# Performance work log

Hardware: AMD Instinct MI355X
Metric: run time of the kernel (lower is better)

Reference implementation:

```python
import jax, jax.numpy as jnp
import numpy as np

N = 200000      # number of nodes / samples
D = 256         # embedding_dim
K = 20          # n_clusters


def setup_inputs() -> dict:
    key = jax.random.key(0)
    k1, k2 = jax.random.split(key)
    embeddings = jax.random.normal(k1, (N, D), dtype=jnp.float32)
    # indicator P has orthonormal-ish columns in the original (top-k eigenvectors
    # of ZZ^T); random values are fine for a correctness baseline of the math.
    indicator = jax.random.normal(k2, (N, K), dtype=jnp.float32)
    return {"embeddings": embeddings, "indicator": indicator}


def reference(embeddings, indicator):
    # Jc = tr(Z Z^T) - tr(P^T Z Z^T P)
    # tr(Z Z^T) = sum(Z * Z)
    term1 = jnp.sum(embeddings * embeddings)
    # tr(P^T Z Z^T P) = || Z^T P ||_F^2 ; Z^T P is [D, K] (tiny), avoids N x N gram.
    ztp = jnp.einsum('nd,nk->dk', embeddings, indicator)
    term2 = jnp.sum(ztp * ztp)
    return term1 - term2
```

## Files before the change

### kernel.cpp

```cpp
#include <hip/hip_runtime.h>

#define NN 200000
#define DD 256
#define KK 20

__global__ __launch_bounds__(512) void egac_main(
    const float* __restrict__ Z, const float* __restrict__ P,
    float* __restrict__ ztp_part, float* __restrict__ t1_part, int chunk) {
  const int t = threadIdx.x;
  const int c2 = t & 127;
  const int r = t >> 7;
  const int b = blockIdx.x;
  const int base = b * chunk;
  int rows = NN - base;
  if (rows > chunk) rows = chunk;

  float acc0[KK], acc1[KK];
#pragma unroll
  for (int k = 0; k < KK; ++k) { acc0[k] = 0.f; acc1[k] = 0.f; }
  float t1 = 0.f;

  const float2* Zb = (const float2*)(Z + (size_t)base * DD);

#pragma unroll 4
  for (int j = r; j < rows; j += 4) {
    float2 zv = Zb[j * (DD / 2) + c2];
    int rowu = __builtin_amdgcn_readfirstlane(base + j);
    const float4* pr = (const float4*)(P + (size_t)rowu * KK);
    float4 pa = pr[0], pb = pr[1], pc = pr[2], pd = pr[3], pe = pr[4];
    float pv[KK] = {pa.x, pa.y, pa.z, pa.w, pb.x, pb.y, pb.z, pb.w,
                    pc.x, pc.y, pc.z, pc.w, pd.x, pd.y, pd.z, pd.w,
                    pe.x, pe.y, pe.z, pe.w};
    t1 += zv.x * zv.x + zv.y * zv.y;
#pragma unroll
    for (int k = 0; k < KK; ++k) {
      acc0[k] += zv.x * pv[k];
      acc1[k] += zv.y * pv[k];
    }
  }

  __shared__ float red[KK][DD];
  __shared__ float wsum[8];
  for (int ph = 0; ph < 4; ++ph) {
    if (r == ph) {
      if (ph == 0) {
#pragma unroll
        for (int k = 0; k < KK; ++k) {
          red[k][2 * c2] = acc0[k];
          red[k][2 * c2 + 1] = acc1[k];
        }
      } else {
#pragma unroll
        for (int k = 0; k < KK; ++k) {
          red[k][2 * c2] += acc0[k];
          red[k][2 * c2 + 1] += acc1[k];
        }
      }
    }
    __syncthreads();
  }

#pragma unroll
  for (int off = 32; off > 0; off >>= 1) t1 += __shfl_xor(t1, off, 64);
  if ((t & 63) == 0) wsum[t >> 6] = t1;
  __syncthreads();

  const float* redf = &red[0][0];
#pragma unroll
  for (int i = 0; i < (KK * DD) / 512; ++i)
    ztp_part[(size_t)b * (KK * DD) + i * 512 + t] = redf[i * 512 + t];
  if (t == 0) {
    float s = 0.f;
#pragma unroll
    for (int w = 0; w < 8; ++w) s += wsum[w];
    t1_part[b] = s;
  }
}

__global__ __launch_bounds__(512) void egac_reduce(
    const float* __restrict__ ztp_part, const float* __restrict__ t1_part,
    float* __restrict__ out, int nb) {
  __shared__ float red[16][32];
  const int t = threadIdx.x;
  const int e_local = t & 31;
  const int psub = t >> 5;
  const int e = blockIdx.x * 32 + e_local;

  float s = 0.f;
#pragma unroll
  for (int j = 0; j < 16; ++j) {
    int p = psub * 16 + j;
    if (p < nb) s += ztp_part[(size_t)p * (KK * DD) + e];
  }
  red[psub][e_local] = s;
  __syncthreads();
  for (int sh = 8; sh >= 1; sh >>= 1) {
    if (psub < sh) red[psub][e_local] += red[psub + sh][e_local];
    __syncthreads();
  }
  if (t == 0) {
    float ssq = 0.f;
#pragma unroll
    for (int i = 0; i < 32; ++i) {
      float v = red[0][i];
      ssq += v * v;
    }
    atomicAdd(out, -ssq);
  }

  if (blockIdx.x == 0) {
    float v = (t < nb) ? t1_part[t] : 0.f;
#pragma unroll
    for (int off = 32; off > 0; off >>= 1) v += __shfl_xor(v, off, 64);
    __shared__ float w2[8];
    if ((t & 63) == 0) w2[t >> 6] = v;
    __syncthreads();
    if (t == 0) {
      float tt = 0.f;
#pragma unroll
      for (int w = 0; w < 8; ++w) tt += w2[w];
      atomicAdd(out, tt);
    }
  }
}

extern "C" void kernel_launch(void* const* d_in, const int* in_sizes, int n_in,
                              void* d_out, int out_size, void* d_ws,
                              size_t ws_size, hipStream_t stream) {
  const float* Z = (const float*)d_in[0];
  const float* P = (const float*)d_in[1];
  float* out = (float*)d_out;

  int nb = 256;
  size_t per_block = (size_t)KK * DD * sizeof(float) + sizeof(float);
  if (ws_size < (size_t)nb * per_block) {
    nb = (int)(ws_size / per_block);
    if (nb < 1) nb = 1;
  }
  float* ztp_part = (float*)d_ws;
  float* t1_part = (float*)d_ws + (size_t)nb * KK * DD;
  int chunk = (NN + nb - 1) / nb;

  hipMemsetAsync(d_out, 0, sizeof(float), stream);
  egac_main<<<nb, 512, 0, stream>>>(Z, P, ztp_part, t1_part, chunk);
  egac_reduce<<<160, 512, 0, stream>>>(ztp_part, t1_part, out, nb);
}
```

Before: 367.8 us.

## Software-pipeline row loads with float4 lanes and rebalance grid to more blocks

The main kernel now processes rows with 256-thread blocks where each wave handles one row using float4 loads per lane. It adds a three-stage register software pipeline that prefetches Z and P rows ahead of the FMA work, which is meant to hide global memory latency. The grid grows from 256 to 1000 blocks so more CUs are filled, and the reduce kernel gains loops to handle the larger partial count. The cost is more register pressure and a larger partial-sum buffer to reduce. The pipeline also assumes chunk divides evenly and silently clamps out-of-range rows to row 0.

After: 321.1 us. 1.15x faster.

```diff
diff --git a/kernel.cpp b/kernel.cpp
--- a/kernel.cpp
+++ b/kernel.cpp
@@ -4,56 +4,87 @@
 #define DD 256
 #define KK 20
 
-__global__ __launch_bounds__(512) void egac_main(
+
+#define STAGE_LOAD(s, zv, Q0, Q1, Q2, Q3, Q4)                              \
+  {                                                                        \
+    int j_ = base + ((s) << 2) + w;                                        \
+    if (j_ > NN - 1) j_ = 0;        \
+    zv = Zr[(size_t)j_ * (DD / 4) + lane];                                 \
+    int ru_ = __builtin_amdgcn_readfirstlane(j_);                          \
+    const float4* pp_ = (const float4*)(P + (size_t)ru_ * KK);             \
+    Q0 = pp_[0]; Q1 = pp_[1]; Q2 = pp_[2]; Q3 = pp_[3]; Q4 = pp_[4];       \
+  }
+
+#define STAGE_COMPUTE(zv, Q0, Q1, Q2, Q3, Q4)                              \
+  {                                                                        \
+    float zz_[4] = {zv.x, zv.y, zv.z, zv.w};                               \
+    float pv_[KK] = {Q0.x, Q0.y, Q0.z, Q0.w, Q1.x, Q1.y, Q1.z, Q1.w,       \
+                     Q2.x, Q2.y, Q2.z, Q2.w, Q3.x, Q3.y, Q3.z, Q3.w,       \
+                     Q4.x, Q4.y, Q4.z, Q4.w};                              \
+    t1 += zz_[0] * zz_[0] + zz_[1] * zz_[1];                               \
+    t1 += zz_[2] * zz_[2] + zz_[3] * zz_[3];                               \
+    _Pragma("unroll") for (int k_ = 0; k_ < KK; ++k_) {                    \
+      _Pragma("unroll") for (int c_ = 0; c_ < 4; ++c_)                     \
+          acc[k_][c_] += zz_[c_] * pv_[k_];                                \
+    }                                                                      \
+  }
+
+__global__ __launch_bounds__(256, 2) void egac_main(
     const float* __restrict__ Z, const float* __restrict__ P,
     float* __restrict__ ztp_part, float* __restrict__ t1_part, int chunk) {
   const int t = threadIdx.x;
-  const int c2 = t & 127;
-  const int r = t >> 7;
+  const int lane = t & 63;
+  const int w = t >> 6;
   const int b = blockIdx.x;
   const int base = b * chunk;
-  int rows = NN - base;
-  if (rows > chunk) rows = chunk;
+  const int nst = chunk >> 2;
 
-  float acc0[KK], acc1[KK];
+  float acc[KK][4];
 #pragma unroll
-  for (int k = 0; k < KK; ++k) { acc0[k] = 0.f; acc1[k] = 0.f; }
+  for (int k = 0; k < KK; ++k)
+#pragma unroll
+    for (int c = 0; c < 4; ++c) acc[k][c] = 0.f;
   float t1 = 0.f;
 
-  const float2* Zb = (const float2*)(Z + (size_t)base * DD);
+  const float4* Zr = (const float4*)Z;
 
-#pragma unroll 4
-  for (int j = r; j < rows; j += 4) {
-    float2 zv = Zb[j * (DD / 2) + c2];
-    int rowu = __builtin_amdgcn_readfirstlane(base + j);
-    const float4* pr = (const float4*)(P + (size_t)rowu * KK);
-    float4 pa = pr[0], pb = pr[1], pc = pr[2], pd = pr[3], pe = pr[4];
-    float pv[KK] = {pa.x, pa.y, pa.z, pa.w, pb.x, pb.y, pb.z, pb.w,
-                    pc.x, pc.y, pc.z, pc.w, pd.x, pd.y, pd.z, pd.w,
-                    pe.x, pe.y, pe.z, pe.w};
-    t1 += zv.x * zv.x + zv.y * zv.y;
-#pragma unroll
-    for (int k = 0; k < KK; ++k) {
-      acc0[k] += zv.x * pv[k];
-      acc1[k] += zv.y * pv[k];
-    }
+  float4 zA, A0, A1, A2, A3, A4;
+  float4 zB, B0, B1, B2, B3, B4;
+  float4 zC, C0, C1, C2, C3, C4;
+
+  STAGE_LOAD(0, zA, A0, A1, A2, A3, A4);
+  STAGE_LOAD(1, zB, B0, B1, B2, B3, B4);
+
+  int s = 0;
+  const int m_end = (nst - 2) / 3;
+  for (int m = 0; m < m_end; ++m) {
+    STAGE_LOAD(s + 2, zC, C0, C1, C2, C3, C4);
+    STAGE_COMPUTE(zA, A0, A1, A2, A3, A4);
+    STAGE_LOAD(s + 3, zA, A0, A1, A2, A3, A4);
+    STAGE_COMPUTE(zB, B0, B1, B2, B3, B4);
+    STAGE_LOAD(s + 4, zB, B0, B1, B2, B3, B4);
+    STAGE_COMPUTE(zC, C0, C1, C2, C3, C4);
+    s += 3;
   }
+  STAGE_COMPUTE(zA, A0, A1, A2, A3, A4);
+  STAGE_COMPUTE(zB, B0, B1, B2, B3, B4);
 
   __shared__ float red[KK][DD];
-  __shared__ float wsum[8];
+  __shared__ float wsum[4];
   for (int ph = 0; ph < 4; ++ph) {
-    if (r == ph) {
+    if (w == ph) {
       if (ph == 0) {
 #pragma unroll
-        for (int k = 0; k < KK; ++k) {
-          red[k][2 * c2] = acc0[k];
-          red[k][2 * c2 + 1] = acc1[k];
-        }
+        for (int k = 0; k < KK; ++k)
+          ((float4*)&red[k][0])[lane] =
+              make_float4(acc[k][0], acc[k][1], acc[k][2], acc[k][3]);
       } else {
 #pragma unroll
         for (int k = 0; k < KK; ++k) {
-          red[k][2 * c2] += acc0[k];
-          red[k][2 * c2 + 1] += acc1[k];
+          float4 r = ((float4*)&red[k][0])[lane];
+          r.x += acc[k][0]; r.y += acc[k][1];
+          r.z += acc[k][2]; r.w += acc[k][3];
+          ((float4*)&red[k][0])[lane] = r;
         }
       }
     }
@@ -62,19 +93,15 @@
 
 #pragma unroll
   for (int off = 32; off > 0; off >>= 1) t1 += __shfl_xor(t1, off, 64);
-  if ((t & 63) == 0) wsum[t >> 6] = t1;
+  if (lane == 0) wsum[w] = t1;
   __syncthreads();
 
-  const float* redf = &red[0][0];
+  float4* dst = (float4*)(ztp_part + (size_t)b * (KK * DD));
+  const float4* src = (const float4*)&red[0][0];
 #pragma unroll
-  for (int i = 0; i < (KK * DD) / 512; ++i)
-    ztp_part[(size_t)b * (KK * DD) + i * 512 + t] = redf[i * 512 + t];
-  if (t == 0) {
-    float s = 0.f;
-#pragma unroll
-    for (int w = 0; w < 8; ++w) s += wsum[w];
-    t1_part[b] = s;
-  }
+  for (int i = 0; i < (KK * DD) / (4 * 256); ++i)
+    dst[i * 256 + t] = src[i * 256 + t];
+  if (t == 0) t1_part[b] = wsum[0] + wsum[1] + wsum[2] + wsum[3];
 }
 
 __global__ __launch_bounds__(512) void egac_reduce(
@@ -82,20 +109,16 @@
     float* __restrict__ out, int nb) {
   __shared__ float red[16][32];
   const int t = threadIdx.x;
-  const int e_local = t & 31;
-  const int psub = t >> 5;
-  const int e = blockIdx.x * 32 + e_local;
+  const int el = t & 31;
+  const int ps = t >> 5;
+  const int e = blockIdx.x * 32 + el;
 
   float s = 0.f;
-#pragma unroll
-  for (int j = 0; j < 16; ++j) {
-    int p = psub * 16 + j;
-    if (p < nb) s += ztp_part[(size_t)p * (KK * DD) + e];
-  }
-  red[psub][e_local] = s;
+  for (int p = ps; p < nb; p += 16) s += ztp_part[(size_t)p * (KK * DD) + e];
+  red[ps][el] = s;
   __syncthreads();
   for (int sh = 8; sh >= 1; sh >>= 1) {
-    if (psub < sh) red[psub][e_local] += red[psub + sh][e_local];
+    if (ps < sh) red[ps][el] += red[ps + sh][el];
     __syncthreads();
   }
   if (t == 0) {
@@ -109,7 +132,8 @@
   }
 
   if (blockIdx.x == 0) {
-    float v = (t < nb) ? t1_part[t] : 0.f;
+    float v = 0.f;
+    for (int i = t; i < nb; i += 512) v += t1_part[i];
 #pragma unroll
     for (int off = 32; off > 0; off >>= 1) v += __shfl_xor(v, off, 64);
     __shared__ float w2[8];
@@ -118,7 +142,7 @@
     if (t == 0) {
       float tt = 0.f;
 #pragma unroll
-      for (int w = 0; w < 8; ++w) tt += w2[w];
+      for (int i = 0; i < 8; ++i) tt += w2[i];
       atomicAdd(out, tt);
     }
   }
@@ -131,17 +155,15 @@
   const float* P = (const float*)d_in[1];
   float* out = (float*)d_out;
 
-  int nb = 256;
-  size_t per_block = (size_t)KK * DD * sizeof(float) + sizeof(float);
-  if (ws_size < (size_t)nb * per_block) {
-    nb = (int)(ws_size / per_block);
-    if (nb < 1) nb = 1;
-  }
+  int nb = 1000;
+  size_t need = (size_t)nb * (KK * DD) * sizeof(float) + (size_t)nb * sizeof(float);
+  if (ws_size < need) nb = 250;
+  int chunk = NN / nb;
+
   float* ztp_part = (float*)d_ws;
   float* t1_part = (float*)d_ws + (size_t)nb * KK * DD;
-  int chunk = (NN + nb - 1) / nb;
 
   hipMemsetAsync(d_out, 0, sizeof(float), stream);
-  egac_main<<<nb, 512, 0, stream>>>(Z, P, ztp_part, t1_part, chunk);
+  egac_main<<<nb, 256, 0, stream>>>(Z, P, ztp_part, t1_part, chunk);
   egac_reduce<<<160, 512, 0, stream>>>(ztp_part, t1_part, out, nb);
 }
```
